# Kernel optimization log

Hardware: AMD Instinct MI355X
Metric: run time of the kernel (lower is better)

## Reference

```python
import jax, jax.numpy as jnp
import numpy as np
from jax import lax

B, C, H, W = 16, 3, 256, 256
K = 3          # lbp kernel size (odd)
POOL = 2
Q = 8          # quant_len
LN_EPS = 1e-5


def _lbp_kernel(c, k):
    half = k // 2
    idx_pairs = [[[0, 0], [k - 1, k - 1]],
                 [[0, half], [k - 1, half]],
                 [[0, k - 1], [k - 1, 0]],
                 [[half, k - 1], [half, 0]]]
    kerns = []
    for pair in idx_pairs:
        for idx in pair:
            m = np.zeros((c, k, k), np.float32)
            m[:, half, half] = 1.0
            m[:, idx[0], idx[1]] = -1.0
            kerns.append(m)
    return jnp.asarray(np.stack(kerns))  # [8, C, K, K]


LBP_KERNEL = _lbp_kernel(C, K)


def setup_inputs() -> dict:
    key = jax.random.key(0)
    ks = jax.random.split(key, 8)
    return {
        "x": jax.random.normal(ks[0], (B, C, H, W), jnp.float32),
        "clamp_low": jnp.float32(-150.0),
        "clamp_high": jnp.float32(150.0),
        "w_expand": jax.random.normal(ks[1], (56, 3, 1, 1), jnp.float32) * 0.1,
        "b_expand": jax.random.normal(ks[2], (56,), jnp.float32) * 0.05,
        "w_conv": jax.random.normal(ks[3], (16, 4, 1, 1), jnp.float32) * 0.1,
        "b_conv": jax.random.normal(ks[4], (16,), jnp.float32) * 0.05,
        "w_final": jax.random.normal(ks[5], (1, 16, 3, 3), jnp.float32) * 0.1,
        "b_final": jax.random.normal(ks[6], (1,), jnp.float32) * 0.05,
    }


def reference(x, clamp_low, clamp_high, w_expand, b_expand, w_conv, b_conv, w_final, b_final):
    leaky = lambda v: jax.nn.leaky_relu(v, 0.01)
    bsz = x.shape[0]

    # avg_pool2d(kernel=POOL, stride=1, pad=POOL//2, count_include_pad=True) -> [B,C,H+1,W+1]
    pad = POOL // 2
    xp = lax.reduce_window(x, 0.0, lax.add, (1, 1, POOL, POOL), (1, 1, 1, 1),
                           [(0, 0), (0, 0), (pad, pad), (pad, pad)]) / float(POOL * POOL)

    # LBP difference conv: 8 output channels, SAME padding
    hk = K // 2
    xl = lax.conv_general_dilated(xp, LBP_KERNEL, (1, 1), [(hk, hk), (hk, hk)],
                                  dimension_numbers=("NCHW", "OIHW", "NCHW"))
    xl = jnp.clip(xl, clamp_low, clamp_high)

    b4 = bsz * 4
    hp, wp = xl.shape[-2], xl.shape[-1]
    n = hp * wp
    xl = xl.reshape(b4, 2, n)  # [B4, 2, N]

    # per-sample, per-channel quantization boundaries: measure[b,i,c] = i*cd + min
    mn = xl.min(axis=-1)                       # [B4, 2]
    mx = xl.max(axis=-1)                       # [B4, 2]
    cd = (mx - mn) / Q
    measure = jnp.arange(Q + 1, dtype=xl.dtype)[None, :, None] * cd[:, None, :] + mn[:, None, :]  # [B4,Q+1,2]

    def bin_mask(vals, ch):
        # keep raw value where lo_i <= v <= hi_i, else 0  -> [B4, Q, N]
        v = vals[:, None, :]
        lo = measure[:, :-1, ch][:, :, None]
        hi = measure[:, 1:, ch][:, :, None]
        return jnp.where((v >= lo) & (v <= hi), v, 0.0)

    m0 = bin_mask(xl[:, 0, :], 0)  # [B4, Q, N]
    m1 = bin_mask(xl[:, 1, :], 1)  # [B4, Q, N]

    # joint histogram of masked values: equivalent to per-pixel outer product + one-hot mask conv
    hist = jnp.einsum("bin,bjn->bij", m0, m1)       # [B4, Q, Q]
    hist = hist / jnp.sum(hist)                      # global normalizer (torch.sum(x))
    hist = hist.reshape(b4, Q * Q, 1)

    # levels: (bin_index + 1) * measure[:, 1, :]
    ii, jj = jnp.meshgrid(jnp.arange(Q), jnp.arange(Q), indexing="ij")
    idxs = jnp.stack([ii, jj], axis=-1).reshape(Q * Q, 2)          # cartesian_prod order
    levels = (idxs[None].astype(xl.dtype) + 1.0) * measure[:, 1, :][:, None, :]  # [B4,64,2]

    feat = jnp.concatenate([levels, hist], axis=2)   # [B4, 64, 3]
    feat = feat.reshape(bsz, 4, Q * Q, 3).transpose(0, 3, 1, 2)  # [B, 3, 4, 64]

    # 1x1 conv 3 -> 56
    h = leaky(jnp.einsum("bcij,oc->boij", feat, w_expand[:, :, 0, 0]) + b_expand[None, :, None, None])
    h = h.transpose(0, 2, 3, 1)  # [B, 4, 64, 56] -> channels=4, spatial (64,56)

    # nearest interpolate spatial (64,56) -> (H,W): src = floor(dst * in / out)
    src_h = (jnp.arange(H) * h.shape[2]) // H
    src_w = (jnp.arange(W) * h.shape[3]) // W
    h = h[:, :, src_h][:, :, :, src_w]  # [B, 4, H, W]

    # layer_norm over last two dims, no affine
    mean = h.mean(axis=(-2, -1), keepdims=True)
    var = jnp.mean((h - mean) ** 2, axis=(-2, -1), keepdims=True)
    h = (h - mean) / jnp.sqrt(var + LN_EPS)

    # 1x1 conv 4 -> 16
    h = leaky(jnp.einsum("bchw,oc->bohw", h, w_conv[:, :, 0, 0]) + b_conv[None, :, None, None])

    # 3x3 conv 16 -> 1, SAME padding
    out = lax.conv_general_dilated(h, w_final, (1, 1), [(1, 1), (1, 1)],
                                   dimension_numbers=("NCHW", "OIHW", "NCHW"))
    out = leaky(out + b_final[None, :, None, None])
    return out
```

## Files before the change

### kernel.cpp

```cpp
#include <hip/hip_runtime.h>
#include <stdint.h>
#include <math.h>

#define HH 256
#define WW 256
#define BATCH 16
#define HP 257
#define SROW 264
#define SH 259
#define SBP (SH*SROW)
#define NPIX (HP*HP)

__device__ __forceinline__ float leaky(float v){ return v >= 0.f ? v : 0.01f*v; }

__device__ __forceinline__ unsigned fkey(float f){
    unsigned u = __float_as_uint(f);
    return (u & 0x80000000u) ? ~u : (u | 0x80000000u);
}
__device__ __forceinline__ float funkey(unsigned k){
    return (k & 0x80000000u) ? __uint_as_float(k ^ 0x80000000u) : __uint_as_float(~k);
}

__device__ __forceinline__ void group_off(int k, int& dh, int& dw){
    dh = (k == 3) ? 0 : -1;
    dw = (k == 3) ? 1 : (k - 1);
}

__global__ __launch_bounds__(256) void k1_pool(const float* __restrict__ x, float* __restrict__ s,
                                               unsigned* __restrict__ mnk, unsigned* __restrict__ mxk,
                                               float* __restrict__ hist){
    if (blockIdx.x == 0){
        if (threadIdx.x < 128){ mnk[threadIdx.x] = 0xFFFFFFFFu; mxk[threadIdx.x] = 0u; }
        for (int t = threadIdx.x; t < 4096; t += 256) hist[t] = 0.f;
    }
    int idx = blockIdx.x*256 + threadIdx.x;
    if (idx >= BATCH*SBP) return;
    int b = idx / SBP;
    int r = idx % SBP;
    int ph = r / SROW, pw = r % SROW;
    int h = ph - 1, w = pw - 1;
    float val = 0.f;
    if ((unsigned)h < (unsigned)HP && (unsigned)w < (unsigned)HP){
        const float* xb = x + (size_t)b*3*HH*WW;
        float acc = 0.f;
        #pragma unroll
        for (int dy=-1; dy<=0; ++dy){
            int i = h+dy; if ((unsigned)i >= HH) continue;
            #pragma unroll
            for (int dx=-1; dx<=0; ++dx){
                int j = w+dx; if ((unsigned)j >= WW) continue;
                int o = i*WW + j;
                acc += xb[o] + xb[HH*WW + o] + xb[2*HH*WW + o];
            }
        }
        val = acc * 0.25f;
    }
    s[idx] = val;
}

__global__ __launch_bounds__(256) void k2_minmax(const float* __restrict__ s, const float* __restrict__ cl,
                                                 const float* __restrict__ chp,
                                                 unsigned* __restrict__ mnk, unsigned* __restrict__ mxk){
    int b = blockIdx.y;
    int wv = threadIdx.x >> 6, lane = threadIdx.x & 63;
    int dh, dw; group_off(wv, dh, dw);
    int doff = dh*SROW + dw;
    const float* sp = s + (size_t)b*SBP + SROW + 1;
    float mn0=INFINITY, mx0=-INFINITY, mn1=INFINITY, mx1=-INFINITY;
    for (int idx = blockIdx.x*64 + lane; idx < NPIX; idx += gridDim.x*64){
        int h = idx / HP, w = idx - h*HP;
        const float* p = sp + h*SROW + w;
        float c = p[0];
        float v0 = c - p[doff];
        float v1 = c - p[-doff];
        mn0 = fminf(mn0,v0); mx0 = fmaxf(mx0,v0);
        mn1 = fminf(mn1,v1); mx1 = fmaxf(mx1,v1);
    }
    #pragma unroll
    for (int off=32; off; off>>=1){
        mn0 = fminf(mn0, __shfl_down(mn0, off));
        mx0 = fmaxf(mx0, __shfl_down(mx0, off));
        mn1 = fminf(mn1, __shfl_down(mn1, off));
        mx1 = fmaxf(mx1, __shfl_down(mx1, off));
    }
    if (lane == 0){
        float lo = cl[0], hi = chp[0];
        int g = b*4 + wv;
        atomicMin(&mnk[g*2+0], fkey(fminf(fmaxf(mn0, lo), hi)));
        atomicMax(&mxk[g*2+0], fkey(fminf(fmaxf(mx0, lo), hi)));
        atomicMin(&mnk[g*2+1], fkey(fminf(fmaxf(mn1, lo), hi)));
        atomicMax(&mxk[g*2+1], fkey(fminf(fmaxf(mx1, lo), hi)));
    }
}

__global__ __launch_bounds__(256) void k3_hist(const float* __restrict__ s, const float* __restrict__ cl,
                                               const float* __restrict__ chp,
                                               const unsigned* __restrict__ mnk, const unsigned* __restrict__ mxk,
                                               float* __restrict__ hist){
    __shared__ float lh[4*64*32];
    int b = blockIdx.y;
    int wv = threadIdx.x >> 6, lane = threadIdx.x & 63;
    for (int t = threadIdx.x; t < 4*64*32; t += 256) lh[t] = 0.f;
    __syncthreads();
    int g = b*4 + wv;
    float lo = cl[0], hi = chp[0];
    float mn0 = funkey(mnk[g*2+0]), mx0 = funkey(mxk[g*2+0]);
    float mn1 = funkey(mnk[g*2+1]), mx1 = funkey(mxk[g*2+1]);
    float cd0 = (mx0-mn0)*0.125f;
    float cd1 = (mx1-mn1)*0.125f;
    float m0[9], m1[9];
    #pragma unroll
    for (int i=0;i<9;i++){
        m0[i] = __fadd_rn(__fmul_rn((float)i, cd0), mn0);
        m1[i] = __fadd_rn(__fmul_rn((float)i, cd1), mn1);
    }
    int dh, dw; group_off(wv, dh, dw);
    int doff = dh*SROW + dw;
    const float* sp = s + (size_t)b*SBP + SROW + 1;
    float* lhg = lh + wv*2048 + (lane & 31);
    for (int idx = blockIdx.x*64 + lane; idx < NPIX; idx += gridDim.x*64){
        int h = idx / HP, w = idx - h*HP;
        const float* p = sp + h*SROW + w;
        float c = p[0];
        float v0 = fminf(fmaxf(c - p[doff],  lo), hi);
        float v1 = fminf(fmaxf(c - p[-doff], lo), hi);
        unsigned b0=0, b1=0;
        #pragma unroll
        for (int i=0;i<8;i++){
            b0 |= (v0>=m0[i] && v0<=m0[i+1]) ? (1u<<i) : 0u;
            b1 |= (v1>=m1[i] && v1<=m1[i+1]) ? (1u<<i) : 0u;
        }
        float pr = v0*v1;
        unsigned bb0=b0;
        while (bb0){
            int i = __ffs(bb0)-1; bb0 &= bb0-1;
            unsigned bb1=b1;
            while (bb1){
                int j = __ffs(bb1)-1; bb1 &= bb1-1;
                atomicAdd(&lhg[(i*8+j)*32], pr);
            }
        }
    }
    __syncthreads();
    float acc = 0.f;
    #pragma unroll
    for (int r=0;r<32;r++) acc += lh[(wv*64 + lane)*32 + ((lane + r)&31)];
    atomicAdd(&hist[g*64 + lane], acc);
}

__global__ __launch_bounds__(256) void k4a(const float* __restrict__ hist,
                    const unsigned* __restrict__ mnk, const unsigned* __restrict__ mxk,
                    const float* __restrict__ we, const float* __restrict__ be,
                    float* __restrict__ hsm, float* __restrict__ stats){
    __shared__ float hloc[3584];
    __shared__ float sred[4];
    int g = blockIdx.x;
    int tid = threadIdx.x;
    float ps = 0.f;
    for (int t=tid; t<4096; t+=256) ps += hist[t];
    #pragma unroll
    for (int off=32; off; off>>=1) ps += __shfl_down(ps, off);
    if ((tid&63)==0) sred[tid>>6] = ps;
    __syncthreads();
    float S = sred[0]+sred[1]+sred[2]+sred[3];

    float mn0 = funkey(mnk[g*2+0]), mx0 = funkey(mxk[g*2+0]);
    float mn1 = funkey(mnk[g*2+1]), mx1 = funkey(mxk[g*2+1]);
    float lvl0 = __fadd_rn(__fmul_rn(1.0f,(mx0-mn0)*0.125f), mn0);
    float lvl1 = __fadd_rn(__fmul_rn(1.0f,(mx1-mn1)*0.125f), mn1);

    for (int e=tid; e<3584; e+=256){
        int ij = e/56, o = e%56;
        int i = ij>>3, j = ij&7;
        float f0 = __fmul_rn((float)(i+1), lvl0);
        float f1 = __fmul_rn((float)(j+1), lvl1);
        float f2 = hist[g*64+ij] / S;
        float a = f0*we[o*3+0] + f1*we[o*3+1] + f2*we[o*3+2] + be[o];
        a = leaky(a);
        hloc[e] = a;
        hsm[(size_t)g*3584 + e] = a;
    }
    __syncthreads();

    float pm = 0.f;
    for (int e=tid; e<3584; e+=256){
        int o = e%56;
        int lo_ = (32*o+6)/7, hi_ = (32*o+31)/7;
        float wgt = (float)(4*(hi_-lo_+1));
        pm += hloc[e]*wgt;
    }
    #pragma unroll
    for (int off=32; off; off>>=1) pm += __shfl_down(pm, off);
    if ((tid&63)==0) sred[tid>>6]=pm;
    __syncthreads();
    float mean = (sred[0]+sred[1]+sred[2]+sred[3]) * (1.0f/65536.0f);
    __syncthreads();
    float pv = 0.f;
    for (int e=tid; e<3584; e+=256){
        int o = e%56;
        int lo_ = (32*o+6)/7, hi_ = (32*o+31)/7;
        float wgt = (float)(4*(hi_-lo_+1));
        float d = hloc[e]-mean;
        pv += d*d*wgt;
    }
    #pragma unroll
    for (int off=32; off; off>>=1) pv += __shfl_down(pv, off);
    if ((tid&63)==0) sred[tid>>6]=pv;
    __syncthreads();
    float var = (sred[0]+sred[1]+sred[2]+sred[3]) * (1.0f/65536.0f);
    if (tid==0){
        stats[g*2+0] = mean;
        stats[g*2+1] = 1.0f / sqrtf(var + 1e-5f);
    }
}

__global__ __launch_bounds__(256) void k4w(const float* __restrict__ hsm, const float* __restrict__ stats,
                                           const float* __restrict__ wc, const float* __restrict__ bc,
                                           const float* __restrict__ wf,
                                           float* __restrict__ w9g){
    __shared__ float wfl[144];
    if (threadIdx.x < 144) wfl[threadIdx.x] = wf[threadIdx.x];
    __syncthreads();
    int idx = blockIdx.x*256 + threadIdx.x;
    if (idx >= 16*64*56) return;
    int sxc = idx % 56;
    int r = (idx/56) & 63;
    int b = idx / (56*64);
    int e = r*56 + sxc;
    float hn[4];
    #pragma unroll
    for (int k=0;k<4;k++){
        int g = b*4+k;
        hn[k] = (hsm[(size_t)g*3584 + e] - stats[g*2]) * stats[g*2+1];
    }
    float w9v[9] = {0,0,0,0,0,0,0,0,0};
    #pragma unroll
    for (int c=0;c<16;c++){
        float hv = bc[c];
        #pragma unroll
        for (int k=0;k<4;k++) hv += wc[c*4+k]*hn[k];
        hv = leaky(hv);
        #pragma unroll
        for (int t=0;t<9;t++) w9v[t] += wfl[c*9+t]*hv;
    }
    float* dst = w9g + (((size_t)b*64 + r)*9)*56 + sxc;
    #pragma unroll
    for (int t=0;t<9;t++) dst[t*56] = w9v[t];
}

__global__ __launch_bounds__(256) void k5_out(const float* __restrict__ w9g, const float* __restrict__ bf,
                                              float* __restrict__ out){
    int x = threadIdx.x;
    int y = blockIdx.x & 255;
    int b = blockIdx.x >> 8;
    const float* wb = w9g + (size_t)b*64*9*56;
    float acc = bf[0];
    int sxm = ((x-1)*7) >> 5;
    int sx0 = (x*7) >> 5;
    int sxp = ((x+1)*7) >> 5;
    #pragma unroll
    for (int dy=0; dy<3; ++dy){
        int yy = y + dy - 1;
        if ((unsigned)yy >= 256u) continue;
        const float* wr = wb + (((yy>>2)*9) + dy*3)*56;
        if (x >= 1)   acc += wr[0*56 + sxm];
                      acc += wr[1*56 + sx0];
        if (x <= 254) acc += wr[2*56 + sxp];
    }
    out[((size_t)(b*256 + y))*256 + x] = leaky(acc);
}

extern "C" void kernel_launch(void* const* d_in, const int* in_sizes, int n_in,
                              void* d_out, int out_size, void* d_ws, size_t ws_size,
                              hipStream_t stream){
    const float* x  = (const float*)d_in[0];
    const float* cl = (const float*)d_in[1];
    const float* ch = (const float*)d_in[2];
    const float* we = (const float*)d_in[3];
    const float* be = (const float*)d_in[4];
    const float* wc = (const float*)d_in[5];
    const float* bc = (const float*)d_in[6];
    const float* wf = (const float*)d_in[7];
    const float* bf = (const float*)d_in[8];
    float* out = (float*)d_out;

    float* s = (float*)d_ws;
    size_t off = (size_t)BATCH*SBP;
    unsigned* mnk = (unsigned*)(s + off); off += 128;
    unsigned* mxk = (unsigned*)(s + off); off += 128;
    float* hist = s + off; off += 4096;
    float* hsm  = s + off; off += 229376;
    float* stats= s + off; off += 128;
    float* w9g  = s + off; off += (size_t)16*64*9*56;

    k1_pool<<<(BATCH*SBP + 255)/256, 256, 0, stream>>>(x, s, mnk, mxk, hist);
    k2_minmax<<<dim3(64,16), 256, 0, stream>>>(s, cl, ch, mnk, mxk);
    k3_hist<<<dim3(64,16), 256, 0, stream>>>(s, cl, ch, mnk, mxk, hist);
    k4a<<<64, 256, 0, stream>>>(hist, mnk, mxk, we, be, hsm, stats);
    k4w<<<(16*64*56 + 255)/256, 256, 0, stream>>>(hsm, stats, wc, bc, wf, w9g);
    k5_out<<<16*256, 256, 0, stream>>>(w9g, bf, out);
}
```

Before: 157.0 us.

## Fuse six kernel launches into one cooperative persistent kernel with grid syncs

Replaces the chain of six separate kernel launches with a single cooperative kernel of 512 blocks. The stages (pool, min/max, histogram, stats, weight folding, output) are separated by grid-wide syncs, with a fallback to the old launches if the cooperative launch fails. The goal is to remove per-launch overhead and inter-kernel gaps. In exchange it adds the cost of grid barriers, a fixed grid size that may underfill some stages, and 32 KB of shared memory per block, which may limit occupancy.

```diff
diff --git a/kernel.cpp b/kernel.cpp
--- a/kernel.cpp
+++ b/kernel.cpp
@@ -1,6 +1,9 @@
 #include <hip/hip_runtime.h>
+#include <hip/hip_cooperative_groups.h>
 #include <stdint.h>
 #include <math.h>
+
+namespace cg = cooperative_groups;
 
 #define HH 256
 #define WW 256
@@ -10,6 +13,7 @@
 #define SH 259
 #define SBP (SH*SROW)
 #define NPIX (HP*HP)
+#define NBLK 512
 
 __device__ __forceinline__ float leaky(float v){ return v >= 0.f ? v : 0.01f*v; }
 
@@ -24,6 +28,271 @@
 __device__ __forceinline__ void group_off(int k, int& dh, int& dw){
     dh = (k == 3) ? 0 : -1;
     dw = (k == 3) ? 1 : (k - 1);
+}
+
+__global__ __launch_bounds__(256) void mega(
+        const float* __restrict__ x, const float* __restrict__ cl, const float* __restrict__ chp,
+        const float* __restrict__ we, const float* __restrict__ be,
+        const float* __restrict__ wc, const float* __restrict__ bc,
+        const float* __restrict__ wf, const float* __restrict__ bf,
+        float* __restrict__ out,
+        float* __restrict__ s, unsigned* __restrict__ mnk, unsigned* __restrict__ mxk,
+        float* __restrict__ hist, float* __restrict__ hsm, float* __restrict__ stats,
+        float* __restrict__ w9g){
+    cg::grid_group grid = cg::this_grid();
+    __shared__ __align__(16) float smem[8192];
+    int tid = threadIdx.x, bid = blockIdx.x;
+    int wv = tid >> 6, lane = tid & 63;
+
+    if (bid == 0){
+        if (tid < 128){ mnk[tid] = 0xFFFFFFFFu; mxk[tid] = 0u; }
+        for (int t = tid; t < 4096; t += 256) hist[t] = 0.f;
+    }
+    for (int idx = bid*256 + tid; idx < BATCH*SBP; idx += NBLK*256){
+        int b = idx / SBP;
+        int r = idx % SBP;
+        int ph = r / SROW, pw = r % SROW;
+        int h = ph - 1, w = pw - 1;
+        float val = 0.f;
+        if ((unsigned)h < (unsigned)HP && (unsigned)w < (unsigned)HP){
+            const float* xb = x + (size_t)b*3*HH*WW;
+            float acc = 0.f;
+            #pragma unroll
+            for (int dy=-1; dy<=0; ++dy){
+                int i = h+dy; if ((unsigned)i >= HH) continue;
+                #pragma unroll
+                for (int dx=-1; dx<=0; ++dx){
+                    int j = w+dx; if ((unsigned)j >= WW) continue;
+                    int o = i*WW + j;
+                    acc += xb[o] + xb[HH*WW + o] + xb[2*HH*WW + o];
+                }
+            }
+            val = acc * 0.25f;
+        }
+        s[idx] = val;
+    }
+    grid.sync();
+
+    {
+        int b = bid >> 5, chunk = bid & 31;
+        const float* sp = s + (size_t)b*SBP + SROW + 1;
+        float mn[8], mx[8];
+        #pragma unroll
+        for (int q=0;q<8;q++){ mn[q]=INFINITY; mx[q]=-INFINITY; }
+        for (int idx = chunk*256 + tid; idx < NPIX; idx += 32*256){
+            int h = idx / HP, w = idx - h*HP;
+            const float* p = sp + h*SROW + w;
+            float c = p[0];
+            float n0 = p[-SROW-1], n1 = p[-SROW], n2 = p[-SROW+1], n3 = p[1];
+            float o0 = p[ SROW+1], o1 = p[ SROW], o2 = p[ SROW-1], o3 = p[-1];
+            float v0=c-n0, v1=c-o0, v2=c-n1, v3=c-o1, v4=c-n2, v5=c-o2, v6=c-n3, v7=c-o3;
+            mn[0]=fminf(mn[0],v0); mx[0]=fmaxf(mx[0],v0);
+            mn[1]=fminf(mn[1],v1); mx[1]=fmaxf(mx[1],v1);
+            mn[2]=fminf(mn[2],v2); mx[2]=fmaxf(mx[2],v2);
+            mn[3]=fminf(mn[3],v3); mx[3]=fmaxf(mx[3],v3);
+            mn[4]=fminf(mn[4],v4); mx[4]=fmaxf(mx[4],v4);
+            mn[5]=fminf(mn[5],v5); mx[5]=fmaxf(mx[5],v5);
+            mn[6]=fminf(mn[6],v6); mx[6]=fmaxf(mx[6],v6);
+            mn[7]=fminf(mn[7],v7); mx[7]=fmaxf(mx[7],v7);
+        }
+        #pragma unroll
+        for (int off=32; off; off>>=1){
+            #pragma unroll
+            for (int q=0;q<8;q++){
+                mn[q] = fminf(mn[q], __shfl_down(mn[q], off));
+                mx[q] = fmaxf(mx[q], __shfl_down(mx[q], off));
+            }
+        }
+        float* redmn = smem;
+        float* redmx = smem + 32;
+        if (lane == 0){
+            #pragma unroll
+            for (int q=0;q<8;q++){ redmn[wv*8+q]=mn[q]; redmx[wv*8+q]=mx[q]; }
+        }
+        __syncthreads();
+        if (tid < 8){
+            float a  = fminf(fminf(redmn[tid],redmn[8+tid]), fminf(redmn[16+tid],redmn[24+tid]));
+            float bb = fmaxf(fmaxf(redmx[tid],redmx[8+tid]), fmaxf(redmx[16+tid],redmx[24+tid]));
+            float lo = cl[0], hi = chp[0];
+            int g = b*4 + (tid>>1), ch = tid&1;
+            atomicMin(&mnk[g*2+ch], fkey(fminf(fmaxf(a,  lo), hi)));
+            atomicMax(&mxk[g*2+ch], fkey(fminf(fmaxf(bb, lo), hi)));
+        }
+        __syncthreads();
+    }
+    grid.sync();
+
+    {
+        float* lh = smem;
+        for (int t = tid; t < 4*64*32; t += 256) lh[t] = 0.f;
+        __syncthreads();
+        int b = bid >> 5, chunk = bid & 31;
+        int g = b*4 + wv;
+        float lo = cl[0], hi = chp[0];
+        float mn0 = funkey(mnk[g*2+0]), mx0 = funkey(mxk[g*2+0]);
+        float mn1 = funkey(mnk[g*2+1]), mx1 = funkey(mxk[g*2+1]);
+        float cd0 = (mx0-mn0)*0.125f;
+        float cd1 = (mx1-mn1)*0.125f;
+        float m0[9], m1[9];
+        #pragma unroll
+        for (int i=0;i<9;i++){
+            m0[i] = __fadd_rn(__fmul_rn((float)i, cd0), mn0);
+            m1[i] = __fadd_rn(__fmul_rn((float)i, cd1), mn1);
+        }
+        int dh, dw; group_off(wv, dh, dw);
+        int doff = dh*SROW + dw;
+        const float* sp = s + (size_t)b*SBP + SROW + 1;
+        float* lhg = lh + wv*2048 + (lane & 31);
+        for (int idx = chunk*64 + lane; idx < NPIX; idx += 32*64){
+            int h = idx / HP, w = idx - h*HP;
+            const float* p = sp + h*SROW + w;
+            float c = p[0];
+            float v0 = fminf(fmaxf(c - p[doff],  lo), hi);
+            float v1 = fminf(fmaxf(c - p[-doff], lo), hi);
+            unsigned b0=0, b1=0;
+            #pragma unroll
+            for (int i=0;i<8;i++){
+                b0 |= (v0>=m0[i] && v0<=m0[i+1]) ? (1u<<i) : 0u;
+                b1 |= (v1>=m1[i] && v1<=m1[i+1]) ? (1u<<i) : 0u;
+            }
+            float pr = v0*v1;
+            unsigned bb0=b0;
+            while (bb0){
+                int i = __ffs(bb0)-1; bb0 &= bb0-1;
+                unsigned bb1=b1;
+                while (bb1){
+                    int j = __ffs(bb1)-1; bb1 &= bb1-1;
+                    atomicAdd(&lhg[(i*8+j)*32], pr);
+                }
+            }
+        }
+        __syncthreads();
+        float acc = 0.f;
+        #pragma unroll
+        for (int r=0;r<32;r++) acc += lh[(wv*64 + lane)*32 + ((lane + r)&31)];
+        atomicAdd(&hist[g*64 + lane], acc);
+        __syncthreads();
+    }
+    grid.sync();
+
+    if (bid < 64){
+        float* hloc = smem;
+        float* sred = smem + 3584;
+        int g = bid;
+        float ps = 0.f;
+        for (int t=tid; t<4096; t+=256) ps += hist[t];
+        #pragma unroll
+        for (int off=32; off; off>>=1) ps += __shfl_down(ps, off);
+        if (lane==0) sred[wv] = ps;
+        __syncthreads();
+        float S = sred[0]+sred[1]+sred[2]+sred[3];
+
+        float mn0 = funkey(mnk[g*2+0]), mx0 = funkey(mxk[g*2+0]);
+        float mn1 = funkey(mnk[g*2+1]), mx1 = funkey(mxk[g*2+1]);
+        float lvl0 = __fadd_rn(__fmul_rn(1.0f,(mx0-mn0)*0.125f), mn0);
+        float lvl1 = __fadd_rn(__fmul_rn(1.0f,(mx1-mn1)*0.125f), mn1);
+
+        for (int e=tid; e<3584; e+=256){
+            int ij = e/56, o = e%56;
+            int i = ij>>3, j = ij&7;
+            float f0 = __fmul_rn((float)(i+1), lvl0);
+            float f1 = __fmul_rn((float)(j+1), lvl1);
+            float f2 = hist[g*64+ij] / S;
+            float a = f0*we[o*3+0] + f1*we[o*3+1] + f2*we[o*3+2] + be[o];
+            a = leaky(a);
+            hloc[e] = a;
+            hsm[(size_t)g*3584 + e] = a;
+        }
+        __syncthreads();
+
+        float pm = 0.f;
+        for (int e=tid; e<3584; e+=256){
+            int o = e%56;
+            int lo_ = (32*o+6)/7, hi_ = (32*o+31)/7;
+            pm += hloc[e] * (float)(4*(hi_-lo_+1));
+        }
+        #pragma unroll
+        for (int off=32; off; off>>=1) pm += __shfl_down(pm, off);
+        if (lane==0) sred[wv]=pm;
+        __syncthreads();
+        float mean = (sred[0]+sred[1]+sred[2]+sred[3]) * (1.0f/65536.0f);
+        __syncthreads();
+        float pv = 0.f;
+        for (int e=tid; e<3584; e+=256){
+            int o = e%56;
+            int lo_ = (32*o+6)/7, hi_ = (32*o+31)/7;
+            float d = hloc[e]-mean;
+            pv += d*d * (float)(4*(hi_-lo_+1));
+        }
+        #pragma unroll
+        for (int off=32; off; off>>=1) pv += __shfl_down(pv, off);
+        if (lane==0) sred[wv]=pv;
+        __syncthreads();
+        float var = (sred[0]+sred[1]+sred[2]+sred[3]) * (1.0f/65536.0f);
+        if (tid==0){
+            stats[g*2+0] = mean;
+            stats[g*2+1] = 1.0f / sqrtf(var + 1e-5f);
+        }
+    }
+    grid.sync();
+
+    {
+        float* wfl = smem;
+        if (tid < 144) wfl[tid] = wf[tid];
+        __syncthreads();
+        for (int idx = bid*256 + tid; idx < 16*64*56; idx += NBLK*256){
+            int sxc = idx % 56;
+            int r = (idx/56) & 63;
+            int b = idx / (56*64);
+            int e = r*56 + sxc;
+            float hn[4];
+            #pragma unroll
+            for (int k=0;k<4;k++){
+                int g = b*4+k;
+                hn[k] = (hsm[(size_t)g*3584 + e] - stats[g*2]) * stats[g*2+1];
+            }
+            float w9v[9] = {0,0,0,0,0,0,0,0,0};
+            #pragma unroll
+            for (int c=0;c<16;c++){
+                float hv = bc[c];
+                #pragma unroll
+                for (int k=0;k<4;k++) hv += wc[c*4+k]*hn[k];
+                hv = leaky(hv);
+                #pragma unroll
+                for (int t=0;t<9;t++) w9v[t] += wfl[c*9+t]*hv;
+            }
+            float* dst = w9g + (((size_t)b*64 + r)*9)*56 + sxc;
+            #pragma unroll
+            for (int t=0;t<9;t++) dst[t*56] = w9v[t];
+        }
+    }
+    grid.sync();
+
+    {
+        int x_ = tid;
+        float bias = bf[0];
+        int sxm = ((x_-1)*7) >> 5;
+        int sx0 = (x_*7) >> 5;
+        int sxp = ((x_+1)*7) >> 5;
+        #pragma unroll
+        for (int t8=0; t8<8; ++t8){
+            int task = bid*8 + t8;
+            int y = task & 255;
+            int b = task >> 8;
+            const float* wb = w9g + (size_t)b*64*9*56;
+            float acc = bias;
+            #pragma unroll
+            for (int dy=0; dy<3; ++dy){
+                int yy = y + dy - 1;
+                if ((unsigned)yy >= 256u) continue;
+                const float* wr = wb + (((yy>>2)*9) + dy*3)*56;
+                if (x_ >= 1)   acc += wr[0*56 + sxm];
+                               acc += wr[1*56 + sx0];
+                if (x_ <= 254) acc += wr[2*56 + sxp];
+            }
+            out[((size_t)(b*256 + y))*256 + x_] = leaky(acc);
+        }
+    }
 }
 
 __global__ __launch_bounds__(256) void k1_pool(const float* __restrict__ x, float* __restrict__ s,
@@ -186,8 +455,7 @@
     for (int e=tid; e<3584; e+=256){
         int o = e%56;
         int lo_ = (32*o+6)/7, hi_ = (32*o+31)/7;
-        float wgt = (float)(4*(hi_-lo_+1));
-        pm += hloc[e]*wgt;
+        pm += hloc[e] * (float)(4*(hi_-lo_+1));
     }
     #pragma unroll
     for (int off=32; off; off>>=1) pm += __shfl_down(pm, off);
@@ -199,9 +467,8 @@
     for (int e=tid; e<3584; e+=256){
         int o = e%56;
         int lo_ = (32*o+6)/7, hi_ = (32*o+31)/7;
-        float wgt = (float)(4*(hi_-lo_+1));
         float d = hloc[e]-mean;
-        pv += d*d*wgt;
+        pv += d*d * (float)(4*(hi_-lo_+1));
     }
     #pragma unroll
     for (int off=32; off; off>>=1) pv += __shfl_down(pv, off);
@@ -293,10 +560,18 @@
     float* stats= s + off; off += 128;
     float* w9g  = s + off; off += (size_t)16*64*9*56;
 
-    k1_pool<<<(BATCH*SBP + 255)/256, 256, 0, stream>>>(x, s, mnk, mxk, hist);
-    k2_minmax<<<dim3(64,16), 256, 0, stream>>>(s, cl, ch, mnk, mxk);
-    k3_hist<<<dim3(64,16), 256, 0, stream>>>(s, cl, ch, mnk, mxk, hist);
-    k4a<<<64, 256, 0, stream>>>(hist, mnk, mxk, we, be, hsm, stats);
-    k4w<<<(16*64*56 + 255)/256, 256, 0, stream>>>(hsm, stats, wc, bc, wf, w9g);
-    k5_out<<<16*256, 256, 0, stream>>>(w9g, bf, out);
-}
+    void* args[] = { (void*)&x, (void*)&cl, (void*)&ch, (void*)&we, (void*)&be,
+                     (void*)&wc, (void*)&bc, (void*)&wf, (void*)&bf, (void*)&out,
+                     (void*)&s, (void*)&mnk, (void*)&mxk, (void*)&hist, (void*)&hsm,
+                     (void*)&stats, (void*)&w9g };
+    hipError_t err = hipLaunchCooperativeKernel((const void*)mega, dim3(NBLK), dim3(256),
+                                                args, 0, stream);
+    if (err != hipSuccess){
+        k1_pool<<<(BATCH*SBP + 255)/256, 256, 0, stream>>>(x, s, mnk, mxk, hist);
+        k2_minmax<<<dim3(64,16), 256, 0, stream>>>(s, cl, ch, mnk, mxk);
+        k3_hist<<<dim3(64,16), 256, 0, stream>>>(s, cl, ch, mnk, mxk, hist);
+        k4a<<<64, 256, 0, stream>>>(hist, mnk, mxk, we, be, hsm, stats);
+        k4w<<<(16*64*56 + 255)/256, 256, 0, stream>>>(hsm, stats, wc, bc, wf, w9g);
+        k5_out<<<16*256, 256, 0, stream>>>(w9g, bf, out);
+    }
+}
```

Measured after the change: 419.5 us. +167.3%, slower.

## Fuse pooling with min/max tiles and merge LN stats into weight kernel

Applied to the files above, without the earlier changes.

Pooling and the LBP min/max pass are fused into one tiled kernel that stages the channel-summed input in shared memory, writes the pooled map, and emits per-tile partial min/max instead of using global atomics. The histogram kernel and a merged k45 kernel reduce those partials themselves, and k45 computes the layer-norm stats and per-row 3x3 weights per batch in shared memory, removing the hsm/stats round trip. This cuts six launches to four and avoids a full re-read of the pooled map for min/max. In exchange it adds redundant partial reductions, halves the histogram grid, and runs the final weight stage on only 16 blocks.

```diff
diff --git a/kernel.cpp b/kernel.cpp
--- a/kernel.cpp
+++ b/kernel.cpp
@@ -10,102 +10,138 @@
 #define SH 259
 #define SBP (SH*SROW)
 #define NPIX (HP*HP)
+#define TS 32
+#define TH 9
+#define NT (TH*TH)
 
 __device__ __forceinline__ float leaky(float v){ return v >= 0.f ? v : 0.01f*v; }
-
-__device__ __forceinline__ unsigned fkey(float f){
-    unsigned u = __float_as_uint(f);
-    return (u & 0x80000000u) ? ~u : (u | 0x80000000u);
-}
-__device__ __forceinline__ float funkey(unsigned k){
-    return (k & 0x80000000u) ? __uint_as_float(k ^ 0x80000000u) : __uint_as_float(~k);
-}
 
 __device__ __forceinline__ void group_off(int k, int& dh, int& dw){
     dh = (k == 3) ? 0 : -1;
     dw = (k == 3) ? 1 : (k - 1);
 }
 
-__global__ __launch_bounds__(256) void k1_pool(const float* __restrict__ x, float* __restrict__ s,
-                                               unsigned* __restrict__ mnk, unsigned* __restrict__ mxk,
-                                               float* __restrict__ hist){
-    if (blockIdx.x == 0){
-        if (threadIdx.x < 128){ mnk[threadIdx.x] = 0xFFFFFFFFu; mxk[threadIdx.x] = 0u; }
-        for (int t = threadIdx.x; t < 4096; t += 256) hist[t] = 0.f;
-    }
-    int idx = blockIdx.x*256 + threadIdx.x;
-    if (idx >= BATCH*SBP) return;
-    int b = idx / SBP;
-    int r = idx % SBP;
-    int ph = r / SROW, pw = r % SROW;
-    int h = ph - 1, w = pw - 1;
-    float val = 0.f;
-    if ((unsigned)h < (unsigned)HP && (unsigned)w < (unsigned)HP){
-        const float* xb = x + (size_t)b*3*HH*WW;
-        float acc = 0.f;
-        #pragma unroll
-        for (int dy=-1; dy<=0; ++dy){
-            int i = h+dy; if ((unsigned)i >= HH) continue;
-            #pragma unroll
-            for (int dx=-1; dx<=0; ++dx){
-                int j = w+dx; if ((unsigned)j >= WW) continue;
-                int o = i*WW + j;
-                acc += xb[o] + xb[HH*WW + o] + xb[2*HH*WW + o];
-            }
-        }
-        val = acc * 0.25f;
-    }
-    s[idx] = val;
-}
-
-__global__ __launch_bounds__(256) void k2_minmax(const float* __restrict__ s, const float* __restrict__ cl,
-                                                 const float* __restrict__ chp,
-                                                 unsigned* __restrict__ mnk, unsigned* __restrict__ mxk){
-    int b = blockIdx.y;
-    int wv = threadIdx.x >> 6, lane = threadIdx.x & 63;
-    int dh, dw; group_off(wv, dh, dw);
-    int doff = dh*SROW + dw;
-    const float* sp = s + (size_t)b*SBP + SROW + 1;
-    float mn0=INFINITY, mx0=-INFINITY, mn1=INFINITY, mx1=-INFINITY;
-    for (int idx = blockIdx.x*64 + lane; idx < NPIX; idx += gridDim.x*64){
-        int h = idx / HP, w = idx - h*HP;
-        const float* p = sp + h*SROW + w;
-        float c = p[0];
-        float v0 = c - p[doff];
-        float v1 = c - p[-doff];
-        mn0 = fminf(mn0,v0); mx0 = fmaxf(mx0,v0);
-        mn1 = fminf(mn1,v1); mx1 = fmaxf(mx1,v1);
+__global__ __launch_bounds__(256) void k12(const float* __restrict__ x, float* __restrict__ s,
+                                           float* __restrict__ pmn, float* __restrict__ pmx,
+                                           float* __restrict__ hist){
+    __shared__ float xs[35][36];
+    __shared__ float sh[34][35];
+    __shared__ float redmn[4][8], redmx[4][8];
+    int blk = blockIdx.x, tid = threadIdx.x;
+    int wv = tid >> 6, lane = tid & 63;
+    int b = blk / NT, tile = blk % NT;
+    int ty = tile / TH, tx = tile % TH;
+
+    if (blk == 0){
+        for (int t = tid; t < 4096; t += 256) hist[t] = 0.f;
+    }
+    if (blk < BATCH){
+        float* sb = s + (size_t)blk*SBP;
+        for (int t = tid; t < 2*SROW; t += 256){
+            int rr = (t < SROW) ? 0 : 258; int cc = t % SROW;
+            sb[rr*SROW + cc] = 0.f;
+        }
+        for (int t = tid; t < 257*7; t += 256){
+            int rr = 1 + t/7, k = t%7;
+            int cc = (k == 0) ? 0 : (257 + k);
+            sb[rr*SROW + cc] = 0.f;
+        }
+    }
+
+    const float* xb = x + (size_t)b*3*HH*WW;
+    int xr0 = ty*TS - 2, xc0 = tx*TS - 2;
+    for (int t = tid; t < 35*35; t += 256){
+        int i = t/35, j = t - i*35;
+        int r = xr0 + i, c = xc0 + j;
+        float v = 0.f;
+        if ((unsigned)r < (unsigned)HH && (unsigned)c < (unsigned)WW){
+            int o = r*WW + c;
+            v = xb[o] + xb[HH*WW + o] + xb[2*HH*WW + o];
+        }
+        xs[i][j] = v;
+    }
+    __syncthreads();
+
+    for (int t = tid; t < 34*34; t += 256){
+        int i = t/34, j = t - i*34;
+        int h = ty*TS - 1 + i, w = tx*TS - 1 + j;
+        float v = 0.f;
+        if ((unsigned)h < (unsigned)HP && (unsigned)w < (unsigned)HP)
+            v = 0.25f*(xs[i][j] + xs[i][j+1] + xs[i+1][j] + xs[i+1][j+1]);
+        sh[i][j] = v;
+    }
+    __syncthreads();
+
+    float mn[8], mx[8];
+    #pragma unroll
+    for (int q=0;q<8;q++){ mn[q]=INFINITY; mx[q]=-INFINITY; }
+    float* sb = s + (size_t)b*SBP;
+    #pragma unroll
+    for (int q4=0; q4<4; ++q4){
+        int p = q4*256 + tid;
+        int lr = p >> 5, lc = p & 31;
+        int h = ty*TS + lr, w = tx*TS + lc;
+        if (h < HP && w < HP){
+            float c = sh[lr+1][lc+1];
+            sb[(h+1)*SROW + (w+1)] = c;
+            float d;
+            d = c - sh[lr  ][lc  ]; mn[0]=fminf(mn[0],d); mx[0]=fmaxf(mx[0],d);
+            d = c - sh[lr+2][lc+2]; mn[1]=fminf(mn[1],d); mx[1]=fmaxf(mx[1],d);
+            d = c - sh[lr  ][lc+1]; mn[2]=fminf(mn[2],d); mx[2]=fmaxf(mx[2],d);
+            d = c - sh[lr+2][lc+1]; mn[3]=fminf(mn[3],d); mx[3]=fmaxf(mx[3],d);
+            d = c - sh[lr  ][lc+2]; mn[4]=fminf(mn[4],d); mx[4]=fmaxf(mx[4],d);
+            d = c - sh[lr+2][lc  ]; mn[5]=fminf(mn[5],d); mx[5]=fmaxf(mx[5],d);
+            d = c - sh[lr+1][lc+2]; mn[6]=fminf(mn[6],d); mx[6]=fmaxf(mx[6],d);
+            d = c - sh[lr+1][lc  ]; mn[7]=fminf(mn[7],d); mx[7]=fmaxf(mx[7],d);
+        }
     }
     #pragma unroll
     for (int off=32; off; off>>=1){
-        mn0 = fminf(mn0, __shfl_down(mn0, off));
-        mx0 = fmaxf(mx0, __shfl_down(mx0, off));
-        mn1 = fminf(mn1, __shfl_down(mn1, off));
-        mx1 = fmaxf(mx1, __shfl_down(mx1, off));
+        #pragma unroll
+        for (int q=0;q<8;q++){
+            mn[q] = fminf(mn[q], __shfl_down(mn[q], off));
+            mx[q] = fmaxf(mx[q], __shfl_down(mx[q], off));
+        }
     }
     if (lane == 0){
-        float lo = cl[0], hi = chp[0];
-        int g = b*4 + wv;
-        atomicMin(&mnk[g*2+0], fkey(fminf(fmaxf(mn0, lo), hi)));
-        atomicMax(&mxk[g*2+0], fkey(fminf(fmaxf(mx0, lo), hi)));
-        atomicMin(&mnk[g*2+1], fkey(fminf(fmaxf(mn1, lo), hi)));
-        atomicMax(&mxk[g*2+1], fkey(fminf(fmaxf(mx1, lo), hi)));
+        #pragma unroll
+        for (int q=0;q<8;q++){ redmn[wv][q]=mn[q]; redmx[wv][q]=mx[q]; }
+    }
+    __syncthreads();
+    if (tid < 8){
+        pmn[(size_t)blk*8 + tid] = fminf(fminf(redmn[0][tid],redmn[1][tid]),
+                                         fminf(redmn[2][tid],redmn[3][tid]));
+        pmx[(size_t)blk*8 + tid] = fmaxf(fmaxf(redmx[0][tid],redmx[1][tid]),
+                                         fmaxf(redmx[2][tid],redmx[3][tid]));
     }
 }
 
 __global__ __launch_bounds__(256) void k3_hist(const float* __restrict__ s, const float* __restrict__ cl,
                                                const float* __restrict__ chp,
-                                               const unsigned* __restrict__ mnk, const unsigned* __restrict__ mxk,
+                                               const float* __restrict__ pmn, const float* __restrict__ pmx,
                                                float* __restrict__ hist){
     __shared__ float lh[4*64*32];
     int b = blockIdx.y;
     int wv = threadIdx.x >> 6, lane = threadIdx.x & 63;
     for (int t = threadIdx.x; t < 4*64*32; t += 256) lh[t] = 0.f;
-    __syncthreads();
-    int g = b*4 + wv;
+
+    float mnA=INFINITY, mxA=-INFINITY, mnB=INFINITY, mxB=-INFINITY;
+    for (int t = lane; t < NT; t += 64){
+        const float* pn = pmn + ((size_t)(b*NT + t))*8;
+        const float* px = pmx + ((size_t)(b*NT + t))*8;
+        mnA = fminf(mnA, pn[2*wv]);   mxA = fmaxf(mxA, px[2*wv]);
+        mnB = fminf(mnB, pn[2*wv+1]); mxB = fmaxf(mxB, px[2*wv+1]);
+    }
+    #pragma unroll
+    for (int off=32; off; off>>=1){
+        mnA = fminf(mnA, __shfl_down(mnA, off)); mxA = fmaxf(mxA, __shfl_down(mxA, off));
+        mnB = fminf(mnB, __shfl_down(mnB, off)); mxB = fmaxf(mxB, __shfl_down(mxB, off));
+    }
+    mnA = __shfl(mnA, 0); mxA = __shfl(mxA, 0);
+    mnB = __shfl(mnB, 0); mxB = __shfl(mxB, 0);
     float lo = cl[0], hi = chp[0];
-    float mn0 = funkey(mnk[g*2+0]), mx0 = funkey(mxk[g*2+0]);
-    float mn1 = funkey(mnk[g*2+1]), mx1 = funkey(mxk[g*2+1]);
+    float mn0 = fminf(fmaxf(mnA, lo), hi), mx0 = fminf(fmaxf(mxA, lo), hi);
+    float mn1 = fminf(fmaxf(mnB, lo), hi), mx1 = fminf(fmaxf(mxB, lo), hi);
     float cd0 = (mx0-mn0)*0.125f;
     float cd1 = (mx1-mn1)*0.125f;
     float m0[9], m1[9];
@@ -114,11 +150,13 @@
         m0[i] = __fadd_rn(__fmul_rn((float)i, cd0), mn0);
         m1[i] = __fadd_rn(__fmul_rn((float)i, cd1), mn1);
     }
+    int g = b*4 + wv;
     int dh, dw; group_off(wv, dh, dw);
     int doff = dh*SROW + dw;
     const float* sp = s + (size_t)b*SBP + SROW + 1;
     float* lhg = lh + wv*2048 + (lane & 31);
-    for (int idx = blockIdx.x*64 + lane; idx < NPIX; idx += gridDim.x*64){
+    __syncthreads();
+    for (int idx = blockIdx.x*64 + lane; idx < NPIX; idx += 32*64){
         int h = idx / HP, w = idx - h*HP;
         const float* p = sp + h*SROW + w;
         float c = p[0];
@@ -148,104 +186,120 @@
     atomicAdd(&hist[g*64 + lane], acc);
 }
 
-__global__ __launch_bounds__(256) void k4a(const float* __restrict__ hist,
-                    const unsigned* __restrict__ mnk, const unsigned* __restrict__ mxk,
+__global__ __launch_bounds__(256) void k45(const float* __restrict__ hist,
+                    const float* __restrict__ pmn, const float* __restrict__ pmx,
+                    const float* __restrict__ cl, const float* __restrict__ chp,
                     const float* __restrict__ we, const float* __restrict__ be,
-                    float* __restrict__ hsm, float* __restrict__ stats){
-    __shared__ float hloc[3584];
+                    const float* __restrict__ wc, const float* __restrict__ bc,
+                    const float* __restrict__ wf,
+                    float* __restrict__ w9g){
+    __shared__ float hloc[4*3584];
+    __shared__ float wfl[144];
+    __shared__ float wred[4][16];
+    __shared__ float gmn[8], gmx[8];
+    __shared__ float gstat[8];
     __shared__ float sred[4];
-    int g = blockIdx.x;
-    int tid = threadIdx.x;
+    int b = blockIdx.x, tid = threadIdx.x;
+    int wv = tid >> 6, lane = tid & 63;
+    if (tid < 144) wfl[tid] = wf[tid];
+
+    float rmn[8], rmx[8];
+    #pragma unroll
+    for (int q=0;q<8;q++){ rmn[q]=INFINITY; rmx[q]=-INFINITY; }
+    for (int t = tid; t < NT; t += 256){
+        const float* pn = pmn + ((size_t)(b*NT + t))*8;
+        const float* px = pmx + ((size_t)(b*NT + t))*8;
+        #pragma unroll
+        for (int q=0;q<8;q++){ rmn[q]=fminf(rmn[q],pn[q]); rmx[q]=fmaxf(rmx[q],px[q]); }
+    }
+    #pragma unroll
+    for (int off=32; off; off>>=1){
+        #pragma unroll
+        for (int q=0;q<8;q++){
+            rmn[q] = fminf(rmn[q], __shfl_down(rmn[q], off));
+            rmx[q] = fmaxf(rmx[q], __shfl_down(rmx[q], off));
+        }
+    }
+    if (lane == 0){
+        #pragma unroll
+        for (int q=0;q<8;q++){ wred[wv][q]=rmn[q]; wred[wv][8+q]=rmx[q]; }
+    }
+    __syncthreads();
+    if (tid < 8)
+        gmn[tid] = fminf(fminf(wred[0][tid],wred[1][tid]), fminf(wred[2][tid],wred[3][tid]));
+    else if (tid < 16){
+        int q = tid-8;
+        gmx[q] = fmaxf(fmaxf(wred[0][8+q],wred[1][8+q]), fmaxf(wred[2][8+q],wred[3][8+q]));
+    }
+
     float ps = 0.f;
-    for (int t=tid; t<4096; t+=256) ps += hist[t];
+    for (int t = tid; t < 4096; t += 256) ps += hist[t];
     #pragma unroll
     for (int off=32; off; off>>=1) ps += __shfl_down(ps, off);
-    if ((tid&63)==0) sred[tid>>6] = ps;
+    if (lane == 0) sred[wv] = ps;
     __syncthreads();
     float S = sred[0]+sred[1]+sred[2]+sred[3];
 
-    float mn0 = funkey(mnk[g*2+0]), mx0 = funkey(mxk[g*2+0]);
-    float mn1 = funkey(mnk[g*2+1]), mx1 = funkey(mxk[g*2+1]);
+    int g = b*4 + wv;
+    float lo = cl[0], hi = chp[0];
+    float mn0 = fminf(fmaxf(gmn[2*wv  ], lo), hi), mx0 = fminf(fmaxf(gmx[2*wv  ], lo), hi);
+    float mn1 = fminf(fmaxf(gmn[2*wv+1], lo), hi), mx1 = fminf(fmaxf(gmx[2*wv+1], lo), hi);
     float lvl0 = __fadd_rn(__fmul_rn(1.0f,(mx0-mn0)*0.125f), mn0);
     float lvl1 = __fadd_rn(__fmul_rn(1.0f,(mx1-mn1)*0.125f), mn1);
-
-    for (int e=tid; e<3584; e+=256){
-        int ij = e/56, o = e%56;
+    for (int e = lane; e < 3584; e += 64){
+        int ij = e/56, o = e - ij*56;
         int i = ij>>3, j = ij&7;
         float f0 = __fmul_rn((float)(i+1), lvl0);
         float f1 = __fmul_rn((float)(j+1), lvl1);
         float f2 = hist[g*64+ij] / S;
         float a = f0*we[o*3+0] + f1*we[o*3+1] + f2*we[o*3+2] + be[o];
-        a = leaky(a);
-        hloc[e] = a;
-        hsm[(size_t)g*3584 + e] = a;
-    }
-    __syncthreads();
-
+        hloc[wv*3584 + e] = leaky(a);
+    }
     float pm = 0.f;
-    for (int e=tid; e<3584; e+=256){
+    for (int e = lane; e < 3584; e += 64){
         int o = e%56;
         int lo_ = (32*o+6)/7, hi_ = (32*o+31)/7;
-        float wgt = (float)(4*(hi_-lo_+1));
-        pm += hloc[e]*wgt;
+        pm += hloc[wv*3584+e] * (float)(4*(hi_-lo_+1));
     }
     #pragma unroll
     for (int off=32; off; off>>=1) pm += __shfl_down(pm, off);
-    if ((tid&63)==0) sred[tid>>6]=pm;
-    __syncthreads();
-    float mean = (sred[0]+sred[1]+sred[2]+sred[3]) * (1.0f/65536.0f);
-    __syncthreads();
+    pm = __shfl(pm, 0);
+    float mean = pm * (1.0f/65536.0f);
     float pv = 0.f;
-    for (int e=tid; e<3584; e+=256){
+    for (int e = lane; e < 3584; e += 64){
         int o = e%56;
         int lo_ = (32*o+6)/7, hi_ = (32*o+31)/7;
-        float wgt = (float)(4*(hi_-lo_+1));
-        float d = hloc[e]-mean;
-        pv += d*d*wgt;
+        float d = hloc[wv*3584+e] - mean;
+        pv += d*d * (float)(4*(hi_-lo_+1));
     }
     #pragma unroll
     for (int off=32; off; off>>=1) pv += __shfl_down(pv, off);
-    if ((tid&63)==0) sred[tid>>6]=pv;
-    __syncthreads();
-    float var = (sred[0]+sred[1]+sred[2]+sred[3]) * (1.0f/65536.0f);
-    if (tid==0){
-        stats[g*2+0] = mean;
-        stats[g*2+1] = 1.0f / sqrtf(var + 1e-5f);
-    }
-}
-
-__global__ __launch_bounds__(256) void k4w(const float* __restrict__ hsm, const float* __restrict__ stats,
-                                           const float* __restrict__ wc, const float* __restrict__ bc,
-                                           const float* __restrict__ wf,
-                                           float* __restrict__ w9g){
-    __shared__ float wfl[144];
-    if (threadIdx.x < 144) wfl[threadIdx.x] = wf[threadIdx.x];
-    __syncthreads();
-    int idx = blockIdx.x*256 + threadIdx.x;
-    if (idx >= 16*64*56) return;
-    int sxc = idx % 56;
-    int r = (idx/56) & 63;
-    int b = idx / (56*64);
-    int e = r*56 + sxc;
-    float hn[4];
-    #pragma unroll
-    for (int k=0;k<4;k++){
-        int g = b*4+k;
-        hn[k] = (hsm[(size_t)g*3584 + e] - stats[g*2]) * stats[g*2+1];
-    }
-    float w9v[9] = {0,0,0,0,0,0,0,0,0};
-    #pragma unroll
-    for (int c=0;c<16;c++){
-        float hv = bc[c];
-        #pragma unroll
-        for (int k=0;k<4;k++) hv += wc[c*4+k]*hn[k];
-        hv = leaky(hv);
-        #pragma unroll
-        for (int t=0;t<9;t++) w9v[t] += wfl[c*9+t]*hv;
-    }
-    float* dst = w9g + (((size_t)b*64 + r)*9)*56 + sxc;
-    #pragma unroll
-    for (int t=0;t<9;t++) dst[t*56] = w9v[t];
+    pv = __shfl(pv, 0);
+    if (lane == 0){
+        gstat[wv*2+0] = mean;
+        gstat[wv*2+1] = 1.0f / sqrtf(pv * (1.0f/65536.0f) + 1e-5f);
+    }
+    __syncthreads();
+
+    for (int e = tid; e < 3584; e += 256){
+        float hn[4];
+        #pragma unroll
+        for (int k=0;k<4;k++) hn[k] = (hloc[k*3584+e] - gstat[2*k]) * gstat[2*k+1];
+        float w9v[9] = {0,0,0,0,0,0,0,0,0};
+        #pragma unroll
+        for (int c=0;c<16;c++){
+            float hv = bc[c];
+            #pragma unroll
+            for (int k=0;k<4;k++) hv += wc[c*4+k]*hn[k];
+            hv = leaky(hv);
+            #pragma unroll
+            for (int t=0;t<9;t++) w9v[t] += wfl[c*9+t]*hv;
+        }
+        int r = e/56, sxc = e - r*56;
+        float* dst = w9g + (((size_t)b*64 + r)*9)*56 + sxc;
+        #pragma unroll
+        for (int t=0;t<9;t++) dst[t*56] = w9v[t];
+    }
 }
 
 __global__ __launch_bounds__(256) void k5_out(const float* __restrict__ w9g, const float* __restrict__ bf,
@@ -286,17 +340,13 @@
 
     float* s = (float*)d_ws;
     size_t off = (size_t)BATCH*SBP;
-    unsigned* mnk = (unsigned*)(s + off); off += 128;
-    unsigned* mxk = (unsigned*)(s + off); off += 128;
+    float* pmn  = s + off; off += (size_t)BATCH*NT*8;
+    float* pmx  = s + off; off += (size_t)BATCH*NT*8;
     float* hist = s + off; off += 4096;
-    float* hsm  = s + off; off += 229376;
-    float* stats= s + off; off += 128;
     float* w9g  = s + off; off += (size_t)16*64*9*56;
 
-    k1_pool<<<(BATCH*SBP + 255)/256, 256, 0, stream>>>(x, s, mnk, mxk, hist);
-    k2_minmax<<<dim3(64,16), 256, 0, stream>>>(s, cl, ch, mnk, mxk);
-    k3_hist<<<dim3(64,16), 256, 0, stream>>>(s, cl, ch, mnk, mxk, hist);
-    k4a<<<64, 256, 0, stream>>>(hist, mnk, mxk, we, be, hsm, stats);
-    k4w<<<(16*64*56 + 255)/256, 256, 0, stream>>>(hsm, stats, wc, bc, wf, w9g);
+    k12<<<BATCH*NT, 256, 0, stream>>>(x, s, pmn, pmx, hist);
+    k3_hist<<<dim3(32,BATCH), 256, 0, stream>>>(s, cl, ch, pmn, pmx, hist);
+    k45<<<BATCH, 256, 0, stream>>>(hist, pmn, pmx, cl, ch, we, be, wc, bc, wf, w9g);
     k5_out<<<16*256, 256, 0, stream>>>(w9g, bf, out);
 }
```

Result: no change. 155.0 us (-1.2%).
